# Kernel optimization log

Hardware: AMD Instinct MI355X
Metric: run time of the kernel (lower is better)

The kernel has to match this reference:

```python
import jax, jax.numpy as jnp
import numpy as np

S, B, H = 512, 128, 1024

def setup_inputs() -> dict:
    key = jax.random.key(0)
    k1, k2, k3, k4 = jax.random.split(key, 4)
    return {
        "hidden": jax.random.normal(k1, (1, B, H), dtype=jnp.float32),
        "encoder_outputs": jax.random.normal(k2, (S, B, H), dtype=jnp.float32),
        "W_attn": jax.random.normal(k3, (H, H), dtype=jnp.float32) * (1.0 / np.sqrt(H)),
        "b_attn": jax.random.normal(k4, (H,), dtype=jnp.float32) * 0.01,
    }

def reference(hidden, encoder_outputs, W_attn, b_attn):
    # 'general' Luong attention: energy_i = h_dec . (W @ enc_i + b)
    # encoder_outputs: [S, B, H]; hidden: [1, B, H]
    energy = jnp.einsum('sbh,kh->sbk', encoder_outputs, W_attn) + b_attn  # [S,B,H]
    scores = jnp.einsum('bh,sbh->bs', hidden[0], energy)                   # [B,S]
    attn = jax.nn.softmax(scores, axis=1)
    return attn[:, None, :]  # [B,1,S]
```

## Files before the change

### kernel.cpp

```cpp
#include <hip/hip_runtime.h>

#define S 512
#define B 128
#define H 1024

#define KG 16
#define KR 64
#define BPG 8
#define BG (B / BPG)

__global__ __launch_bounds__(256) void calc_u_part(const float* __restrict__ hidden,
                                                   const float* __restrict__ W,
                                                   float* __restrict__ part) {
    const int t  = threadIdx.x;
    const int kg = blockIdx.x & (KG - 1);
    const int bg = blockIdx.x >> 4;
    const int b0 = bg * BPG;
    const int h4 = t * 4;
    const int k0 = kg * KR;

    float4 acc[BPG];
#pragma unroll
    for (int j = 0; j < BPG; ++j) acc[j] = make_float4(0.f, 0.f, 0.f, 0.f);

#pragma unroll 8
    for (int kk = 0; kk < KR; ++kk) {
        const int k = k0 + kk;
        const float4 w = *reinterpret_cast<const float4*>(W + (size_t)k * H + h4);
#pragma unroll
        for (int j = 0; j < BPG; ++j) {
            const float hb = hidden[(size_t)(b0 + j) * H + k];
            acc[j].x = fmaf(hb, w.x, acc[j].x);
            acc[j].y = fmaf(hb, w.y, acc[j].y);
            acc[j].z = fmaf(hb, w.z, acc[j].z);
            acc[j].w = fmaf(hb, w.w, acc[j].w);
        }
    }
#pragma unroll
    for (int j = 0; j < BPG; ++j)
        *reinterpret_cast<float4*>(part + ((size_t)kg * B + (b0 + j)) * H + h4) = acc[j];
}

__global__ __launch_bounds__(256) void calc_u_reduce(const float* __restrict__ part,
                                                     float* __restrict__ u) {
    const int idx4 = blockIdx.x * 256 + threadIdx.x;
    const float4* __restrict__ p4 = reinterpret_cast<const float4*>(part);
    float4 s = p4[idx4];
#pragma unroll
    for (int kg = 1; kg < KG; ++kg) {
        float4 v = p4[(size_t)kg * (B * H / 4) + idx4];
        s.x += v.x; s.y += v.y; s.z += v.z; s.w += v.w;
    }
    reinterpret_cast<float4*>(u)[idx4] = s;
}

__global__ __launch_bounds__(256) void calc_u_fallback(const float* __restrict__ hidden,
                                                       const float* __restrict__ W,
                                                       float* __restrict__ u) {
    const int h  = (blockIdx.x & 3) * 256 + threadIdx.x;
    const int bb = blockIdx.x >> 2;
    const float* __restrict__ h0p = hidden + (size_t)bb * H;
    const float* __restrict__ h1p = hidden + (size_t)(bb + 64) * H;
    float acc0 = 0.f, acc1 = 0.f;
#pragma unroll 16
    for (int k = 0; k < H; ++k) {
        float w = W[(size_t)k * H + h];
        acc0 = fmaf(h0p[k], w, acc0);
        acc1 = fmaf(h1p[k], w, acc1);
    }
    u[(size_t)bb * H + h] = acc0;
    u[(size_t)(bb + 64) * H + h] = acc1;
}

__global__ __launch_bounds__(256) void calc_scores(const float* __restrict__ enc,
                                                   const float* __restrict__ u,
                                                   float* __restrict__ scores) {
    const int wid  = threadIdx.x >> 6;
    const int lane = threadIdx.x & 63;
    const int w  = blockIdx.x * 4 + wid;
    const int b  = w & (B - 1);
    const int sg = w >> 7;
    const int s0 = sg * 8;

    const float4* __restrict__ u4 = reinterpret_cast<const float4*>(u + (size_t)b * H);
    const float4 uu0 = u4[lane];
    const float4 uu1 = u4[64 + lane];
    const float4 uu2 = u4[128 + lane];
    const float4 uu3 = u4[192 + lane];

    float acc[8];
#pragma unroll
    for (int j = 0; j < 8; ++j) {
        const float4* __restrict__ e4 =
            reinterpret_cast<const float4*>(enc + ((size_t)(s0 + j) * B + b) * H);
        const float4 e0 = e4[lane];
        const float4 e1 = e4[64 + lane];
        const float4 e2 = e4[128 + lane];
        const float4 e3 = e4[192 + lane];
        float a = e0.x * uu0.x + e0.y * uu0.y + e0.z * uu0.z + e0.w * uu0.w;
        a = fmaf(e1.x, uu1.x, a); a = fmaf(e1.y, uu1.y, a);
        a = fmaf(e1.z, uu1.z, a); a = fmaf(e1.w, uu1.w, a);
        a = fmaf(e2.x, uu2.x, a); a = fmaf(e2.y, uu2.y, a);
        a = fmaf(e2.z, uu2.z, a); a = fmaf(e2.w, uu2.w, a);
        a = fmaf(e3.x, uu3.x, a); a = fmaf(e3.y, uu3.y, a);
        a = fmaf(e3.z, uu3.z, a); a = fmaf(e3.w, uu3.w, a);
        acc[j] = a;
    }
#pragma unroll
    for (int j = 0; j < 8; ++j)
#pragma unroll
        for (int off = 32; off >= 1; off >>= 1)
            acc[j] += __shfl_xor(acc[j], off, 64);

    if (lane == 0) {
        float4* sp = reinterpret_cast<float4*>(scores + (size_t)b * S + s0);
        sp[0] = make_float4(acc[0], acc[1], acc[2], acc[3]);
        sp[1] = make_float4(acc[4], acc[5], acc[6], acc[7]);
    }
}

__global__ __launch_bounds__(256) void softmax_rows(const float* __restrict__ scores,
                                                    float* __restrict__ out) {
    const int b = blockIdx.x;
    const int t = threadIdx.x;
    const int wid = t >> 6, lane = t & 63;
    const float* __restrict__ row = scores + (size_t)b * S;
    float v0 = row[t];
    float v1 = row[t + 256];

    __shared__ float sm[4], ss[4];

    float m = fmaxf(v0, v1);
#pragma unroll
    for (int off = 32; off >= 1; off >>= 1)
        m = fmaxf(m, __shfl_xor(m, off, 64));
    if (lane == 0) sm[wid] = m;
    __syncthreads();
    m = fmaxf(fmaxf(sm[0], sm[1]), fmaxf(sm[2], sm[3]));

    float e0 = __expf(v0 - m);
    float e1 = __expf(v1 - m);
    float sum = e0 + e1;
#pragma unroll
    for (int off = 32; off >= 1; off >>= 1)
        sum += __shfl_xor(sum, off, 64);
    if (lane == 0) ss[wid] = sum;
    __syncthreads();
    sum = ss[0] + ss[1] + ss[2] + ss[3];

    const float inv = 1.f / sum;
    out[(size_t)b * S + t]       = e0 * inv;
    out[(size_t)b * S + t + 256] = e1 * inv;
}

extern "C" void kernel_launch(void* const* d_in, const int* in_sizes, int n_in,
                              void* d_out, int out_size, void* d_ws, size_t ws_size,
                              hipStream_t stream) {
    const float* hidden = (const float*)d_in[0];
    const float* enc    = (const float*)d_in[1];
    const float* W      = (const float*)d_in[2];

    float* u      = (float*)d_ws;
    float* scores = u + (size_t)B * H;
    float* part   = scores + (size_t)B * S;
    float* out    = (float*)d_out;

    const size_t need_full =
        ((size_t)B * H + (size_t)B * S + (size_t)KG * B * H) * sizeof(float);
    if (ws_size >= need_full) {
        calc_u_part  <<<KG * BG, 256, 0, stream>>>(hidden, W, part);
        calc_u_reduce<<<(B * H / 4) / 256, 256, 0, stream>>>(part, u);
    } else {
        calc_u_fallback<<<256, 256, 0, stream>>>(hidden, W, u);
    }
    calc_scores <<<2048, 256, 0, stream>>>(enc, u, scores);
    softmax_rows<<<128,  256, 0, stream>>>(scores, out);
}
```

Baseline: 61.00 us.

## Fuse split-K partial GEMV and reduction into one kernel via shared memory

Result: slower. 67.51 us (+10.7%).

```diff
diff --git a/kernel.cpp b/kernel.cpp
--- a/kernel.cpp
+++ b/kernel.cpp
@@ -4,31 +4,28 @@
 #define B 128
 #define H 1024
 
-#define KG 16
-#define KR 64
-#define BPG 8
-#define BG (B / BPG)
+__global__ __launch_bounds__(256) void calc_u_fused(const float* __restrict__ hidden,
+                                                    const float* __restrict__ W,
+                                                    float* __restrict__ u) {
+    const int t  = threadIdx.x;
+    const int th = t & 15;
+    const int kg = t >> 4;
+    const int bg = blockIdx.x & 15;
+    const int ht = blockIdx.x >> 4;
+    const int b0 = bg * 8;
+    const int h0 = ht * 64 + th * 4;
+    const int k0 = kg * 64;
 
-__global__ __launch_bounds__(256) void calc_u_part(const float* __restrict__ hidden,
-                                                   const float* __restrict__ W,
-                                                   float* __restrict__ part) {
-    const int t  = threadIdx.x;
-    const int kg = blockIdx.x & (KG - 1);
-    const int bg = blockIdx.x >> 4;
-    const int b0 = bg * BPG;
-    const int h4 = t * 4;
-    const int k0 = kg * KR;
+    float4 acc[8];
+#pragma unroll
+    for (int j = 0; j < 8; ++j) acc[j] = make_float4(0.f, 0.f, 0.f, 0.f);
 
-    float4 acc[BPG];
+#pragma unroll 4
+    for (int kk = 0; kk < 64; ++kk) {
+        const int k = k0 + kk;
+        const float4 w = *reinterpret_cast<const float4*>(W + (size_t)k * H + h0);
 #pragma unroll
-    for (int j = 0; j < BPG; ++j) acc[j] = make_float4(0.f, 0.f, 0.f, 0.f);
-
-#pragma unroll 8
-    for (int kk = 0; kk < KR; ++kk) {
-        const int k = k0 + kk;
-        const float4 w = *reinterpret_cast<const float4*>(W + (size_t)k * H + h4);
-#pragma unroll
-        for (int j = 0; j < BPG; ++j) {
+        for (int j = 0; j < 8; ++j) {
             const float hb = hidden[(size_t)(b0 + j) * H + k];
             acc[j].x = fmaf(hb, w.x, acc[j].x);
             acc[j].y = fmaf(hb, w.y, acc[j].y);
@@ -36,40 +33,24 @@
             acc[j].w = fmaf(hb, w.w, acc[j].w);
         }
     }
+
+    __shared__ float red[16][8][64];
 #pragma unroll
-    for (int j = 0; j < BPG; ++j)
-        *reinterpret_cast<float4*>(part + ((size_t)kg * B + (b0 + j)) * H + h4) = acc[j];
-}
+    for (int j = 0; j < 8; ++j)
+        *reinterpret_cast<float4*>(&red[kg][j][th * 4]) = acc[j];
+    __syncthreads();
 
-__global__ __launch_bounds__(256) void calc_u_reduce(const float* __restrict__ part,
-                                                     float* __restrict__ u) {
-    const int idx4 = blockIdx.x * 256 + threadIdx.x;
-    const float4* __restrict__ p4 = reinterpret_cast<const float4*>(part);
-    float4 s = p4[idx4];
+    if (t < 128) {
+        const int b  = t >> 4;
+        const int hq = (t & 15) * 4;
+        float4 s = *reinterpret_cast<const float4*>(&red[0][b][hq]);
 #pragma unroll
-    for (int kg = 1; kg < KG; ++kg) {
-        float4 v = p4[(size_t)kg * (B * H / 4) + idx4];
-        s.x += v.x; s.y += v.y; s.z += v.z; s.w += v.w;
+        for (int g = 1; g < 16; ++g) {
+            const float4 v = *reinterpret_cast<const float4*>(&red[g][b][hq]);
+            s.x += v.x; s.y += v.y; s.z += v.z; s.w += v.w;
+        }
+        *reinterpret_cast<float4*>(u + (size_t)(b0 + b) * H + ht * 64 + hq) = s;
     }
-    reinterpret_cast<float4*>(u)[idx4] = s;
-}
-
-__global__ __launch_bounds__(256) void calc_u_fallback(const float* __restrict__ hidden,
-                                                       const float* __restrict__ W,
-                                                       float* __restrict__ u) {
-    const int h  = (blockIdx.x & 3) * 256 + threadIdx.x;
-    const int bb = blockIdx.x >> 2;
-    const float* __restrict__ h0p = hidden + (size_t)bb * H;
-    const float* __restrict__ h1p = hidden + (size_t)(bb + 64) * H;
-    float acc0 = 0.f, acc1 = 0.f;
-#pragma unroll 16
-    for (int k = 0; k < H; ++k) {
-        float w = W[(size_t)k * H + h];
-        acc0 = fmaf(h0p[k], w, acc0);
-        acc1 = fmaf(h1p[k], w, acc1);
-    }
-    u[(size_t)bb * H + h] = acc0;
-    u[(size_t)(bb + 64) * H + h] = acc1;
 }
 
 __global__ __launch_bounds__(256) void calc_scores(const float* __restrict__ enc,
@@ -162,17 +143,9 @@
 
     float* u      = (float*)d_ws;
     float* scores = u + (size_t)B * H;
-    float* part   = scores + (size_t)B * S;
     float* out    = (float*)d_out;
 
-    const size_t need_full =
-        ((size_t)B * H + (size_t)B * S + (size_t)KG * B * H) * sizeof(float);
-    if (ws_size >= need_full) {
-        calc_u_part  <<<KG * BG, 256, 0, stream>>>(hidden, W, part);
-        calc_u_reduce<<<(B * H / 4) / 256, 256, 0, stream>>>(part, u);
-    } else {
-        calc_u_fallback<<<256, 256, 0, stream>>>(hidden, W, u);
-    }
+    calc_u_fused<<<256,  256, 0, stream>>>(hidden, W, u);
     calc_scores <<<2048, 256, 0, stream>>>(enc, u, scores);
     softmax_rows<<<128,  256, 0, stream>>>(scores, out);
 }
```
